# Kernel tuning notes

Hardware: AMD Instinct MI355X
Metric: run time of the kernel (lower is better)

## Reference

```python
import jax, jax.numpy as jnp
import numpy as np
import math

V, T, D_POI, D_OUT = 200000, 512, 256, 512
D_IN = D_POI + 4
D_HID = D_POI + 100


def setup_inputs() -> dict:
    key = jax.random.key(0)
    ks = jax.random.split(key, 12)
    s = 0.02
    return {
        "prev_poi_idx": jax.random.randint(ks[0], (T,), 0, V),
        "prev_time_frac": jax.random.uniform(ks[1], (T,), jnp.float32),
        "poi_final_emb": jax.random.normal(ks[2], (V, D_POI), jnp.float32),
        "poi_latlon_deg": jax.random.uniform(ks[3], (V, 2), jnp.float32) * 90.0,
        "ln_w": jnp.ones((D_IN,), jnp.float32),
        "ln_b": jnp.zeros((D_IN,), jnp.float32),
        "w1": jax.random.normal(ks[4], (D_IN, D_HID), jnp.float32) * s,
        "b1": jnp.zeros((D_HID,), jnp.float32),
        "w2": jax.random.normal(ks[5], (D_HID, D_POI), jnp.float32) * s,
        "b2": jnp.zeros((D_POI,), jnp.float32),
        "w_ih": jax.random.normal(ks[6], (3 * D_OUT, D_POI), jnp.float32) * s,
        "w_hh": jax.random.normal(ks[7], (3 * D_OUT, D_OUT), jnp.float32) * s,
        "b_ih": jnp.zeros((3 * D_OUT,), jnp.float32),
        "b_hh": jnp.zeros((3 * D_OUT,), jnp.float32),
        "q": jax.random.normal(ks[8], (D_OUT,), jnp.float32),
        "log_lam": jnp.array(0.0, jnp.float32),  # log(recency_lambda=1.0)
    }


def _haversine_km(lat1, lon1, lat2, lon2, eps=1e-12):
    dlat = (lat2 - lat1) * 0.5
    dlon = (lon2 - lon1) * 0.5
    a = jnp.sin(dlat) ** 2 + jnp.clip(jnp.cos(lat1), -1, 1) * jnp.clip(jnp.cos(lat2), -1, 1) * jnp.sin(dlon) ** 2
    c = 2.0 * jnp.arctan2(jnp.sqrt(jnp.clip(a, 0, 1)), jnp.sqrt(jnp.clip(1 - a, eps, 1)))
    return 6371.0088 * c


def _forward(prev_poi_idx, prev_time_frac, poi_final_emb, poi_latlon_deg,
             ln_w, ln_b, w1, b1, w2, b2, w_ih, w_hh, b_ih, b_hh, q, log_lam):
    Tn = prev_poi_idx.shape[0]
    poi_emb = poi_final_emb[prev_poi_idx]                       # (T, d_poi)
    t = jnp.clip(prev_time_frac, 0.0, 1.0)
    sin_t = jnp.sin(2.0 * math.pi * t)
    cos_t = jnp.cos(2.0 * math.pi * t)
    dif = jnp.mod(t[1:] - t[:-1], 1.0) * 24.0
    dt_h = jnp.concatenate([jnp.zeros((1,), t.dtype), dif])
    # _poi_radians is under no_grad in torch
    latlon = jax.lax.stop_gradient(poi_latlon_deg[prev_poi_idx])
    lat = jnp.deg2rad(jnp.clip(latlon[:, 0], -90, 90))
    lon = jnp.deg2rad(jnp.clip(latlon[:, 1], -180, 180))
    dd = _haversine_km(lat[:-1], lon[:-1], lat[1:], lon[1:])
    dd_km = jnp.concatenate([jnp.zeros((1,), dd.dtype), dd])
    feat = jnp.stack([sin_t, cos_t, jnp.log1p(dt_h), jnp.log1p(dd_km)], axis=-1)  # (T, 4)
    x = jnp.concatenate([poi_emb, feat], axis=-1)               # (T, d_poi+4)
    # fuse: LayerNorm -> Linear -> GELU -> (Dropout eval=id) -> Linear
    mu = jnp.mean(x, axis=-1, keepdims=True)
    var = jnp.mean((x - mu) ** 2, axis=-1, keepdims=True)
    x = (x - mu) * jax.lax.rsqrt(var + 1e-5) * ln_w + ln_b
    x = jax.nn.gelu(x @ w1 + b1, approximate=False) @ w2 + b2   # (T, d_poi)
    # GRU (single layer, unidirectional), torch gate order r,z,n
    gi_all = x @ w_ih.T + b_ih                                  # (T, 3H)
    def step(h, gi):
        gh = h @ w_hh.T + b_hh
        gi_r, gi_z, gi_n = jnp.split(gi, 3)
        gh_r, gh_z, gh_n = jnp.split(gh, 3)
        r = jax.nn.sigmoid(gi_r + gh_r)
        z = jax.nn.sigmoid(gi_z + gh_z)
        n = jnp.tanh(gi_n + r * gh_n)
        h_new = (1.0 - z) * n + z * h
        return h_new, h_new
    h0 = jnp.zeros((D_OUT,), x.dtype)
    _, hs = jax.lax.scan(step, h0, gi_all)                      # (T, d_out)
    D = hs.shape[-1]
    score = hs @ (q[:D] / jnp.sqrt(jnp.asarray(D, hs.dtype)))
    age = jnp.arange(Tn, dtype=hs.dtype)
    lam = jnp.maximum(jnp.exp(log_lam), 1e-4)
    score = score - lam * (Tn - 1 - age)
    attn = jax.nn.softmax(score, axis=0)
    summary = jnp.sum(attn[:, None] * hs, axis=0, keepdims=True)  # (1, d_out)
    return summary, attn


def reference(prev_poi_idx, prev_time_frac, poi_final_emb, poi_latlon_deg,
              ln_w, ln_b, w1, b1, w2, b2, w_ih, w_hh, b_ih, b_hh, q, log_lam):
    return _forward(prev_poi_idx, prev_time_frac, poi_final_emb, poi_latlon_deg,
                    ln_w, ln_b, w1, b1, w2, b2, w_ih, w_hh, b_ih, b_hh, q, log_lam)
```

## Files before the change

### kernel.cpp

```cpp
#include <hip/hip_runtime.h>
#include <math.h>

#define TT 512
#define DPOI 256
#define DIN 260
#define DHID 356
#define DOUTD 512
#define G3 1536

#define GB 8
#define HU (DOUTD / GB)
#define NRR (3 * HU)
#define NPAY DOUTD

__global__ __launch_bounds__(512)
void pre_kernel(const int* __restrict__ idx, const float* __restrict__ timef,
                const float* __restrict__ latlon, const float* __restrict__ emb,
                const float* __restrict__ lnw, const float* __restrict__ lnb,
                const float* __restrict__ w1, const float* __restrict__ b1,
                const float* __restrict__ w2, const float* __restrict__ b2,
                const float* __restrict__ wih, const float* __restrict__ bih,
                float* __restrict__ gi, unsigned* __restrict__ hcz) {
    int t = blockIdx.x;
    int tid = threadIdx.x;
    int wave = tid >> 6, lane = tid & 63;

    __shared__ float xl[DIN];
    __shared__ float h1l[DHID];
    __shared__ alignas(16) float x2l[DPOI];
    __shared__ float red[8];
    __shared__ float mu_s, rs_s;

    hcz[(size_t)t * 512 + tid] = 0u;

    float tv = fminf(fmaxf(timef[t], 0.f), 1.f);
    const float TWO_PI = 6.28318530717958647692f;
    float f0 = sinf(TWO_PI * tv);
    float f1 = cosf(TWO_PI * tv);
    float f2 = 0.f, f3 = 0.f;
    if (t > 0) {
        float tp = fminf(fmaxf(timef[t - 1], 0.f), 1.f);
        float d = tv - tp;
        d = d - floorf(d);
        f2 = log1pf(d * 24.f);
        int i0 = idx[t - 1], i1 = idx[t];
        float la0 = latlon[2 * (size_t)i0], lo0 = latlon[2 * (size_t)i0 + 1];
        float la1 = latlon[2 * (size_t)i1], lo1 = latlon[2 * (size_t)i1 + 1];
        const float D2R = 0.01745329251994329577f;
        float lat1 = fminf(fmaxf(la0, -90.f), 90.f) * D2R;
        float lon1 = fminf(fmaxf(lo0, -180.f), 180.f) * D2R;
        float lat2 = fminf(fmaxf(la1, -90.f), 90.f) * D2R;
        float lon2 = fminf(fmaxf(lo1, -180.f), 180.f) * D2R;
        float dlat = (lat2 - lat1) * 0.5f, dlon = (lon2 - lon1) * 0.5f;
        float sdlat = sinf(dlat), sdlon = sinf(dlon);
        float a = sdlat * sdlat +
                  fminf(fmaxf(cosf(lat1), -1.f), 1.f) * fminf(fmaxf(cosf(lat2), -1.f), 1.f) * sdlon * sdlon;
        float aa = fminf(fmaxf(a, 0.f), 1.f);
        float bb = fminf(fmaxf(1.f - a, 1e-12f), 1.f);
        float cc = 2.f * atan2f(sqrtf(aa), sqrtf(bb));
        f3 = log1pf(6371.0088f * cc);
    }
    float fv = (tid == 0) ? f0 : (tid == 1) ? f1 : (tid == 2) ? f2 : f3;

    float v0 = (tid < 256) ? emb[(size_t)idx[t] * DPOI + tid] : 0.f;
    float v1 = (tid < 4) ? fv : 0.f;

    float s = v0 + v1;
    for (int o = 32; o; o >>= 1) s += __shfl_down(s, o, 64);
    if (lane == 0) red[wave] = s;
    __syncthreads();
    if (tid == 0) {
        float mm = 0.f;
        for (int i = 0; i < 8; ++i) mm += red[i];
        mu_s = mm * (1.f / 260.f);
    }
    __syncthreads();
    float mu = mu_s;
    float d0 = (tid < 256) ? (v0 - mu) : 0.f;
    float d1 = (tid < 4) ? (v1 - mu) : 0.f;
    float sq = d0 * d0 + d1 * d1;
    for (int o = 32; o; o >>= 1) sq += __shfl_down(sq, o, 64);
    __syncthreads();
    if (lane == 0) red[wave] = sq;
    __syncthreads();
    if (tid == 0) {
        float vv = 0.f;
        for (int i = 0; i < 8; ++i) vv += red[i];
        rs_s = rsqrtf(vv * (1.f / 260.f) + 1e-5f);
    }
    __syncthreads();
    float rs = rs_s;
    if (tid < 256) xl[tid] = d0 * rs * lnw[tid] + lnb[tid];
    if (tid < 4)   xl[256 + tid] = d1 * rs * lnw[256 + tid] + lnb[256 + tid];
    __syncthreads();

    if (tid < DHID) {
        float acc = b1[tid];
        #pragma unroll 4
        for (int k = 0; k < DIN; ++k) acc = fmaf(xl[k], w1[k * DHID + tid], acc);
        h1l[tid] = 0.5f * acc * (1.f + erff(acc * 0.70710678118654752440f));
    }
    __syncthreads();

    if (tid < DPOI) {
        float acc = b2[tid];
        #pragma unroll 4
        for (int k = 0; k < DHID; ++k) acc = fmaf(h1l[k], w2[k * DPOI + tid], acc);
        x2l[tid] = acc;
    }
    __syncthreads();

    float4 xv = ((const float4*)x2l)[lane];
    for (int r = wave; r < G3; r += 8) {
        float4 wv = ((const float4*)(wih + (size_t)r * DPOI))[lane];
        float sd = xv.x * wv.x + xv.y * wv.y + xv.z * wv.z + xv.w * wv.w;
        for (int o = 32; o; o >>= 1) sd += __shfl_down(sd, o, 64);
        if (lane == 0) gi[(size_t)t * G3 + r] = sd + bih[r];
    }
}

__global__ __launch_bounds__(1024)
void gru_kernel(const float* __restrict__ gi, const float* __restrict__ whh,
                const float* __restrict__ bhh, float* __restrict__ hs,
                unsigned* __restrict__ hcomm) {
    __shared__ alignas(16) float hprev[DOUTD];
    __shared__ float gsum[NRR];

    int b = blockIdx.x;
    int tid = threadIdx.x;
    int wave = tid >> 6, lane = tid & 63;
    int jbase = b * HU;
    int g4 = lane >> 4, l4 = lane & 15;
    int rr0 = wave * 12 + g4 * 3;

    float4 wf0[8], wf1[8], wf2[8];
    float bl0, bl1, bl2;
    {
        int r0 = rr0, r1 = rr0 + 1, r2 = rr0 + 2;
        const float4* p0 = (const float4*)(whh + (size_t)((r0 >> 6) * DOUTD + jbase + (r0 & 63)) * DOUTD);
        const float4* p1 = (const float4*)(whh + (size_t)((r1 >> 6) * DOUTD + jbase + (r1 & 63)) * DOUTD);
        const float4* p2 = (const float4*)(whh + (size_t)((r2 >> 6) * DOUTD + jbase + (r2 & 63)) * DOUTD);
        #pragma unroll
        for (int m = 0; m < 8; ++m) {
            wf0[m] = p0[m * 16 + l4];
            wf1[m] = p1[m * 16 + l4];
            wf2[m] = p2[m * 16 + l4];
        }
        bl0 = bhh[(r0 >> 6) * DOUTD + jbase + (r0 & 63)];
        bl1 = bhh[(r1 >> 6) * DOUTD + jbase + (r1 & 63)];
        bl2 = bhh[(r2 >> 6) * DOUTD + jbase + (r2 & 63)];
    }
    if (tid < DOUTD) hprev[tid] = 0.f;
    __syncthreads();

    const float4* hp4 = (const float4*)hprev;
    long budget = 3000;

    float gir = 0.f, giz = 0.f, gin = 0.f, hreg = 0.f;
    if (tid < HU) {
        int j = jbase + tid;
        gir = gi[j];
        giz = gi[DOUTD + j];
        gin = gi[2 * DOUTD + j];
    }

    for (int s = 0; s < TT; ++s) {
        unsigned pa = 0, pb = 0;
        if (s > 0) {
            if (wave >= 4 && wave < 12 && (wave - 4) != b) {
                int u = ((wave - 4) << 6) + lane;
                const unsigned* ap = hcomm + (size_t)(s - 1) * NPAY + u;
                unsigned tag = (unsigned)s & 0xffffu;
                asm volatile("global_load_dword %0, %1, off sc0 sc1"
                             : "=v"(pa) : "v"(ap) : "memory");
                float xx = (float)(lane + 1) * 1e-6f;
                #pragma unroll
                for (int q = 0; q < 256; ++q) xx = fmaf(xx, 1.0000002f, 1.1920929e-7f);
                asm volatile("global_load_dword %0, %1, off sc0 sc1"
                             : "=v"(pb) : "v"(ap), "v"(xx) : "memory");
                do {
                    unsigned tmp; int scnt;
                    asm volatile(
                        "s_movk_i32 %[cnt], 64\n\t"
                        "1:\n\t"
                        "s_waitcnt vmcnt(1)\n\t"
                        "v_and_b32 %[t], 0xffff, %[pa]\n\t"
                        "v_cmp_ne_u32 vcc, %[tag], %[t]\n\t"
                        "s_cbranch_vccz 9f\n\t"
                        "global_load_dword %[pa], %[ptr], off sc0 sc1\n\t"
                        "s_waitcnt vmcnt(1)\n\t"
                        "v_and_b32 %[t], 0xffff, %[pb]\n\t"
                        "v_cmp_ne_u32 vcc, %[tag], %[t]\n\t"
                        "s_cbranch_vccz 8f\n\t"
                        "global_load_dword %[pb], %[ptr], off sc0 sc1\n\t"
                        "s_sub_u32 %[cnt], %[cnt], 1\n\t"
                        "s_cmp_lg_u32 %[cnt], 0\n\t"
                        "s_cbranch_scc1 1b\n\t"
                        "s_branch 9f\n\t"
                        "8:\n\t"
                        "v_mov_b32 %[pa], %[pb]\n\t"
                        "9:\n\t"
                        : [pa]"+v"(pa), [pb]"+v"(pb), [t]"=&v"(tmp), [cnt]"=&s"(scnt)
                        : [ptr]"v"(ap), [tag]"s"(tag)
                        : "vcc", "scc", "memory");
                    if ((pa & 0xffffu) == tag) break;
                } while (--budget > 0);
                hprev[u] = __uint_as_float(pa & 0xffff0000u);
            }
            __syncthreads();
            asm volatile("" :: "v"(pa), "v"(pb));
        }

        float a0 = 0.f, a1 = 0.f, a2 = 0.f;
        #pragma unroll
        for (int m = 0; m < 8; ++m) {
            float4 h4 = hp4[m * 16 + l4];
            a0 = fmaf(wf0[m].x, h4.x, a0); a0 = fmaf(wf0[m].y, h4.y, a0);
            a0 = fmaf(wf0[m].z, h4.z, a0); a0 = fmaf(wf0[m].w, h4.w, a0);
            a1 = fmaf(wf1[m].x, h4.x, a1); a1 = fmaf(wf1[m].y, h4.y, a1);
            a1 = fmaf(wf1[m].z, h4.z, a1); a1 = fmaf(wf1[m].w, h4.w, a1);
            a2 = fmaf(wf2[m].x, h4.x, a2); a2 = fmaf(wf2[m].y, h4.y, a2);
            a2 = fmaf(wf2[m].z, h4.z, a2); a2 = fmaf(wf2[m].w, h4.w, a2);
        }
        #pragma unroll
        for (int o = 1; o < 16; o <<= 1) {
            a0 += __shfl_xor(a0, o, 64);
            a1 += __shfl_xor(a1, o, 64);
            a2 += __shfl_xor(a2, o, 64);
        }
        if (l4 == 0) {
            gsum[rr0]     = a0 + bl0;
            gsum[rr0 + 1] = a1 + bl1;
            gsum[rr0 + 2] = a2 + bl2;
        }
        __syncthreads();

        if (tid < HU) {
            float gr  = gir + gsum[tid];
            float gz  = giz + gsum[HU + tid];
            float ghn = gsum[2 * HU + tid];
            float r = __builtin_amdgcn_rcpf(1.f + __expf(-gr));
            float z = __builtin_amdgcn_rcpf(1.f + __expf(-gz));
            float xt = gin + r * ghn;
            float n = 1.f - 2.f * __builtin_amdgcn_rcpf(__expf(2.f * xt) + 1.f);
            float hn = (1.f - z) * n + z * hreg;
            hreg = hn;
            unsigned ub = __float_as_uint(hn);
            ub += 0x7fffu + ((ub >> 16) & 1u);
            unsigned pay = (ub & 0xffff0000u) | ((unsigned)(s + 1) & 0xffffu);
            __hip_atomic_store(&hcomm[(size_t)s * NPAY + jbase + tid], pay,
                               __ATOMIC_RELAXED, __HIP_MEMORY_SCOPE_AGENT);
            int j = jbase + tid;
            hs[(size_t)s * DOUTD + j] = hn;
            hprev[j] = hn;
            if (s + 1 < TT) {
                const float* gn = gi + (size_t)(s + 1) * G3;
                gir = gn[j]; giz = gn[DOUTD + j]; gin = gn[2 * DOUTD + j];
            }
        }
    }
}

__global__ void attn_kernel(const float* __restrict__ hs, const float* __restrict__ q,
                            const float* __restrict__ log_lam, float* __restrict__ out) {
    int tid = threadIdx.x;
    int wave = tid >> 6, lane = tid & 63;
    __shared__ float sc[TT];
    __shared__ float at[TT];
    __shared__ float red[8];
    __shared__ float red2[8];
    __shared__ float denom_s, mx_s;

    const float qscale = 0.04419417382415921757f;
    for (int r = wave; r < TT; r += 8) {
        float acc = 0.f;
        #pragma unroll
        for (int m = 0; m < 8; ++m) {
            int k = lane + 64 * m;
            acc = fmaf(hs[(size_t)r * DOUTD + k], q[k], acc);
        }
        for (int o = 32; o; o >>= 1) acc += __shfl_down(acc, o, 64);
        if (lane == 0) sc[r] = acc * qscale;
    }
    __syncthreads();
    float lam = fmaxf(expf(log_lam[0]), 1e-4f);
    float s_i = sc[tid] - lam * (float)(TT - 1 - tid);

    float mval = s_i;
    for (int o = 32; o; o >>= 1) mval = fmaxf(mval, __shfl_down(mval, o, 64));
    if (lane == 0) red[wave] = mval;
    __syncthreads();
    if (tid == 0) {
        float mm = red[0];
        for (int i = 1; i < 8; ++i) mm = fmaxf(mm, red[i]);
        mx_s = mm;
    }
    __syncthreads();
    float e = expf(s_i - mx_s);
    float ssum = e;
    for (int o = 32; o; o >>= 1) ssum += __shfl_down(ssum, o, 64);
    if (lane == 0) red2[wave] = ssum;
    __syncthreads();
    if (tid == 0) {
        float dsum = 0.f;
        for (int i = 0; i < 8; ++i) dsum += red2[i];
        denom_s = dsum;
    }
    __syncthreads();
    float attn = e / denom_s;
    out[DOUTD + tid] = attn;
    at[tid] = attn;
    __syncthreads();
    float acc = 0.f;
    for (int i = 0; i < TT; ++i) acc = fmaf(at[i], hs[(size_t)i * DOUTD + tid], acc);
    out[tid] = acc;
}

extern "C" void kernel_launch(void* const* d_in, const int* in_sizes, int n_in,
                              void* d_out, int out_size, void* d_ws, size_t ws_size,
                              hipStream_t stream) {
    const int*   idx    = (const int*)d_in[0];
    const float* timef  = (const float*)d_in[1];
    const float* emb    = (const float*)d_in[2];
    const float* latlon = (const float*)d_in[3];
    const float* lnw    = (const float*)d_in[4];
    const float* lnb    = (const float*)d_in[5];
    const float* w1     = (const float*)d_in[6];
    const float* b1     = (const float*)d_in[7];
    const float* w2     = (const float*)d_in[8];
    const float* b2     = (const float*)d_in[9];
    const float* wih    = (const float*)d_in[10];
    const float* whh    = (const float*)d_in[11];
    const float* bih    = (const float*)d_in[12];
    const float* bhh    = (const float*)d_in[13];
    const float* q      = (const float*)d_in[14];
    const float* loglam = (const float*)d_in[15];
    float* out = (float*)d_out;

    unsigned* hcomm = (unsigned*)d_ws;
    float* gi = (float*)(hcomm + (size_t)TT * NPAY);
    float* hs = gi + (size_t)TT * G3;

    pre_kernel<<<TT, 512, 0, stream>>>(idx, timef, latlon, emb, lnw, lnb,
                                       w1, b1, w2, b2, wih, bih, gi, hcomm);
    gru_kernel<<<GB, 1024, 0, stream>>>(gi, whh, bhh, hs, hcomm);
    attn_kernel<<<1, TT, 0, stream>>>(hs, q, loglam, out);
}
```

Measured before the change: 1.536 ms.

## Fuse input projection and GRU into one kernel with per-step ready flags

Merges the per-timestep preprocessing (layernorm, MLP, input-gate projection) and the GRU recurrence into one launch. Blocks 0-7 run the recurrence while 256 extra blocks each produce two timesteps of gate inputs and publish per-step ready flags. The recurrence spins on a flag before reading each step's inputs, so preprocessing overlaps the serial scan instead of running before it. A separate init kernel zeroes the comm buffer and flags. This relies on the recurrence blocks and producer blocks being co-resident, uses bounded spin loops with a break that could read stale data, and adds waitcnt fixes in the polling asm.

```diff
diff --git a/kernel.cpp b/kernel.cpp
--- a/kernel.cpp
+++ b/kernel.cpp
@@ -12,123 +12,142 @@
 #define HU (DOUTD / GB)
 #define NRR (3 * HU)
 #define NPAY DOUTD
-
-__global__ __launch_bounds__(512)
-void pre_kernel(const int* __restrict__ idx, const float* __restrict__ timef,
-                const float* __restrict__ latlon, const float* __restrict__ emb,
-                const float* __restrict__ lnw, const float* __restrict__ lnb,
-                const float* __restrict__ w1, const float* __restrict__ b1,
-                const float* __restrict__ w2, const float* __restrict__ b2,
-                const float* __restrict__ wih, const float* __restrict__ bih,
-                float* __restrict__ gi, unsigned* __restrict__ hcz) {
-    int t = blockIdx.x;
+#define PREB 256
+#define NZ4 ((TT * NPAY + TT) / 4)
+
+__global__ void init_kernel(uint4* __restrict__ p) {
+    int i = blockIdx.x * blockDim.x + threadIdx.x;
+    int stride = gridDim.x * blockDim.x;
+    uint4 z; z.x = 0u; z.y = 0u; z.z = 0u; z.w = 0u;
+    for (; i < NZ4; i += stride) p[i] = z;
+}
+
+__global__ __launch_bounds__(1024)
+void mega_kernel(const int* __restrict__ idx, const float* __restrict__ timef,
+                 const float* __restrict__ latlon, const float* __restrict__ emb,
+                 const float* __restrict__ lnw, const float* __restrict__ lnb,
+                 const float* __restrict__ w1, const float* __restrict__ b1,
+                 const float* __restrict__ w2, const float* __restrict__ b2,
+                 const float* __restrict__ wih, const float* __restrict__ bih,
+                 const float* __restrict__ whh, const float* __restrict__ bhh,
+                 float* __restrict__ gi, float* __restrict__ hs,
+                 unsigned* __restrict__ hcomm, unsigned* __restrict__ ready) {
     int tid = threadIdx.x;
     int wave = tid >> 6, lane = tid & 63;
 
-    __shared__ float xl[DIN];
-    __shared__ float h1l[DHID];
-    __shared__ alignas(16) float x2l[DPOI];
-    __shared__ float red[8];
-    __shared__ float mu_s, rs_s;
-
-    hcz[(size_t)t * 512 + tid] = 0u;
-
-    float tv = fminf(fmaxf(timef[t], 0.f), 1.f);
-    const float TWO_PI = 6.28318530717958647692f;
-    float f0 = sinf(TWO_PI * tv);
-    float f1 = cosf(TWO_PI * tv);
-    float f2 = 0.f, f3 = 0.f;
-    if (t > 0) {
-        float tp = fminf(fmaxf(timef[t - 1], 0.f), 1.f);
-        float d = tv - tp;
-        d = d - floorf(d);
-        f2 = log1pf(d * 24.f);
-        int i0 = idx[t - 1], i1 = idx[t];
-        float la0 = latlon[2 * (size_t)i0], lo0 = latlon[2 * (size_t)i0 + 1];
-        float la1 = latlon[2 * (size_t)i1], lo1 = latlon[2 * (size_t)i1 + 1];
-        const float D2R = 0.01745329251994329577f;
-        float lat1 = fminf(fmaxf(la0, -90.f), 90.f) * D2R;
-        float lon1 = fminf(fmaxf(lo0, -180.f), 180.f) * D2R;
-        float lat2 = fminf(fmaxf(la1, -90.f), 90.f) * D2R;
-        float lon2 = fminf(fmaxf(lo1, -180.f), 180.f) * D2R;
-        float dlat = (lat2 - lat1) * 0.5f, dlon = (lon2 - lon1) * 0.5f;
-        float sdlat = sinf(dlat), sdlon = sinf(dlon);
-        float a = sdlat * sdlat +
-                  fminf(fmaxf(cosf(lat1), -1.f), 1.f) * fminf(fmaxf(cosf(lat2), -1.f), 1.f) * sdlon * sdlon;
-        float aa = fminf(fmaxf(a, 0.f), 1.f);
-        float bb = fminf(fmaxf(1.f - a, 1e-12f), 1.f);
-        float cc = 2.f * atan2f(sqrtf(aa), sqrtf(bb));
-        f3 = log1pf(6371.0088f * cc);
-    }
-    float fv = (tid == 0) ? f0 : (tid == 1) ? f1 : (tid == 2) ? f2 : f3;
-
-    float v0 = (tid < 256) ? emb[(size_t)idx[t] * DPOI + tid] : 0.f;
-    float v1 = (tid < 4) ? fv : 0.f;
-
-    float s = v0 + v1;
-    for (int o = 32; o; o >>= 1) s += __shfl_down(s, o, 64);
-    if (lane == 0) red[wave] = s;
-    __syncthreads();
-    if (tid == 0) {
-        float mm = 0.f;
-        for (int i = 0; i < 8; ++i) mm += red[i];
-        mu_s = mm * (1.f / 260.f);
-    }
-    __syncthreads();
-    float mu = mu_s;
-    float d0 = (tid < 256) ? (v0 - mu) : 0.f;
-    float d1 = (tid < 4) ? (v1 - mu) : 0.f;
-    float sq = d0 * d0 + d1 * d1;
-    for (int o = 32; o; o >>= 1) sq += __shfl_down(sq, o, 64);
-    __syncthreads();
-    if (lane == 0) red[wave] = sq;
-    __syncthreads();
-    if (tid == 0) {
-        float vv = 0.f;
-        for (int i = 0; i < 8; ++i) vv += red[i];
-        rs_s = rsqrtf(vv * (1.f / 260.f) + 1e-5f);
-    }
-    __syncthreads();
-    float rs = rs_s;
-    if (tid < 256) xl[tid] = d0 * rs * lnw[tid] + lnb[tid];
-    if (tid < 4)   xl[256 + tid] = d1 * rs * lnw[256 + tid] + lnb[256 + tid];
-    __syncthreads();
-
-    if (tid < DHID) {
-        float acc = b1[tid];
-        #pragma unroll 4
-        for (int k = 0; k < DIN; ++k) acc = fmaf(xl[k], w1[k * DHID + tid], acc);
-        h1l[tid] = 0.5f * acc * (1.f + erff(acc * 0.70710678118654752440f));
-    }
-    __syncthreads();
-
-    if (tid < DPOI) {
-        float acc = b2[tid];
-        #pragma unroll 4
-        for (int k = 0; k < DHID; ++k) acc = fmaf(h1l[k], w2[k * DPOI + tid], acc);
-        x2l[tid] = acc;
-    }
-    __syncthreads();
-
-    float4 xv = ((const float4*)x2l)[lane];
-    for (int r = wave; r < G3; r += 8) {
-        float4 wv = ((const float4*)(wih + (size_t)r * DPOI))[lane];
-        float sd = xv.x * wv.x + xv.y * wv.y + xv.z * wv.z + xv.w * wv.w;
-        for (int o = 32; o; o >>= 1) sd += __shfl_down(sd, o, 64);
-        if (lane == 0) gi[(size_t)t * G3 + r] = sd + bih[r];
-    }
-}
-
-__global__ __launch_bounds__(1024)
-void gru_kernel(const float* __restrict__ gi, const float* __restrict__ whh,
-                const float* __restrict__ bhh, float* __restrict__ hs,
-                unsigned* __restrict__ hcomm) {
+    if (blockIdx.x >= GB) {
+        __shared__ float xl[DIN];
+        __shared__ float h1l[DHID];
+        __shared__ alignas(16) float x2l[DPOI];
+        __shared__ float red[16];
+        __shared__ float mu_s, rs_s;
+        int pb = blockIdx.x - GB;
+
+        for (int half = 0; half < 2; ++half) {
+            int t = pb * 2 + half;
+
+            float fv = 0.f;
+            if (tid < 4) {
+                float tv = fminf(fmaxf(timef[t], 0.f), 1.f);
+                const float TWO_PI = 6.28318530717958647692f;
+                float f0 = sinf(TWO_PI * tv);
+                float f1 = cosf(TWO_PI * tv);
+                float f2 = 0.f, f3 = 0.f;
+                if (t > 0) {
+                    float tp = fminf(fmaxf(timef[t - 1], 0.f), 1.f);
+                    float d = tv - tp;
+                    d = d - floorf(d);
+                    f2 = log1pf(d * 24.f);
+                    int i0 = idx[t - 1], i1 = idx[t];
+                    float la0 = latlon[2 * (size_t)i0], lo0 = latlon[2 * (size_t)i0 + 1];
+                    float la1 = latlon[2 * (size_t)i1], lo1 = latlon[2 * (size_t)i1 + 1];
+                    const float D2R = 0.01745329251994329577f;
+                    float lat1 = fminf(fmaxf(la0, -90.f), 90.f) * D2R;
+                    float lon1 = fminf(fmaxf(lo0, -180.f), 180.f) * D2R;
+                    float lat2 = fminf(fmaxf(la1, -90.f), 90.f) * D2R;
+                    float lon2 = fminf(fmaxf(lo1, -180.f), 180.f) * D2R;
+                    float dlat = (lat2 - lat1) * 0.5f, dlon = (lon2 - lon1) * 0.5f;
+                    float sdlat = sinf(dlat), sdlon = sinf(dlon);
+                    float a = sdlat * sdlat +
+                              fminf(fmaxf(cosf(lat1), -1.f), 1.f) * fminf(fmaxf(cosf(lat2), -1.f), 1.f) * sdlon * sdlon;
+                    float aa = fminf(fmaxf(a, 0.f), 1.f);
+                    float bb = fminf(fmaxf(1.f - a, 1e-12f), 1.f);
+                    float cc = 2.f * atan2f(sqrtf(aa), sqrtf(bb));
+                    f3 = log1pf(6371.0088f * cc);
+                }
+                fv = (tid == 0) ? f0 : (tid == 1) ? f1 : (tid == 2) ? f2 : f3;
+            }
+
+            float v0 = (tid < 256) ? emb[(size_t)idx[t] * DPOI + tid] : 0.f;
+            float v1 = (tid < 4) ? fv : 0.f;
+
+            float s = v0 + v1;
+            for (int o = 32; o; o >>= 1) s += __shfl_down(s, o, 64);
+            if (lane == 0) red[wave] = s;
+            __syncthreads();
+            if (tid == 0) {
+                float mm = 0.f;
+                for (int i = 0; i < 16; ++i) mm += red[i];
+                mu_s = mm * (1.f / 260.f);
+            }
+            __syncthreads();
+            float mu = mu_s;
+            float d0 = (tid < 256) ? (v0 - mu) : 0.f;
+            float d1 = (tid < 4) ? (v1 - mu) : 0.f;
+            float sq = d0 * d0 + d1 * d1;
+            for (int o = 32; o; o >>= 1) sq += __shfl_down(sq, o, 64);
+            __syncthreads();
+            if (lane == 0) red[wave] = sq;
+            __syncthreads();
+            if (tid == 0) {
+                float vv = 0.f;
+                for (int i = 0; i < 16; ++i) vv += red[i];
+                rs_s = rsqrtf(vv * (1.f / 260.f) + 1e-5f);
+            }
+            __syncthreads();
+            float rs = rs_s;
+            if (tid < 256) xl[tid] = d0 * rs * lnw[tid] + lnb[tid];
+            if (tid < 4)   xl[256 + tid] = d1 * rs * lnw[256 + tid] + lnb[256 + tid];
+            __syncthreads();
+
+            if (tid < DHID) {
+                float acc = b1[tid];
+                #pragma unroll 4
+                for (int k = 0; k < DIN; ++k) acc = fmaf(xl[k], w1[k * DHID + tid], acc);
+                h1l[tid] = 0.5f * acc * (1.f + erff(acc * 0.70710678118654752440f));
+            }
+            __syncthreads();
+
+            if (tid < DPOI) {
+                float acc = b2[tid];
+                #pragma unroll 4
+                for (int k = 0; k < DHID; ++k) acc = fmaf(h1l[k], w2[k * DPOI + tid], acc);
+                x2l[tid] = acc;
+            }
+            __syncthreads();
+
+            float4 xv = ((const float4*)x2l)[lane];
+            for (int r = wave; r < G3; r += 16) {
+                float4 wv = ((const float4*)(wih + (size_t)r * DPOI))[lane];
+                float sd = xv.x * wv.x + xv.y * wv.y + xv.z * wv.z + xv.w * wv.w;
+                for (int o = 32; o; o >>= 1) sd += __shfl_down(sd, o, 64);
+                if (lane == 0)
+                    __hip_atomic_store(&gi[(size_t)t * G3 + r], sd + bih[r],
+                                       __ATOMIC_RELAXED, __HIP_MEMORY_SCOPE_AGENT);
+            }
+            __syncthreads();
+            if (tid == 0)
+                __hip_atomic_store(&ready[t], 1u, __ATOMIC_RELAXED,
+                                   __HIP_MEMORY_SCOPE_AGENT);
+            __syncthreads();
+        }
+        return;
+    }
+
     __shared__ alignas(16) float hprev[DOUTD];
     __shared__ float gsum[NRR];
 
     int b = blockIdx.x;
-    int tid = threadIdx.x;
-    int wave = tid >> 6, lane = tid & 63;
     int jbase = b * HU;
     int g4 = lane >> 4, l4 = lane & 15;
     int rr0 = wave * 12 + g4 * 3;
@@ -155,17 +174,22 @@
 
     const float4* hp4 = (const float4*)hprev;
     long budget = 3000;
+    long rbudget = 1000000;
 
     float gir = 0.f, giz = 0.f, gin = 0.f, hreg = 0.f;
     if (tid < HU) {
+        while (__hip_atomic_load(&ready[0], __ATOMIC_RELAXED,
+                                 __HIP_MEMORY_SCOPE_AGENT) == 0u) {
+            if (--rbudget < 0) break;
+        }
         int j = jbase + tid;
-        gir = gi[j];
-        giz = gi[DOUTD + j];
-        gin = gi[2 * DOUTD + j];
+        gir = __hip_atomic_load(&gi[j], __ATOMIC_RELAXED, __HIP_MEMORY_SCOPE_AGENT);
+        giz = __hip_atomic_load(&gi[DOUTD + j], __ATOMIC_RELAXED, __HIP_MEMORY_SCOPE_AGENT);
+        gin = __hip_atomic_load(&gi[2 * DOUTD + j], __ATOMIC_RELAXED, __HIP_MEMORY_SCOPE_AGENT);
     }
 
     for (int s = 0; s < TT; ++s) {
-        unsigned pa = 0, pb = 0;
+        unsigned pa = 0, pb2 = 0;
         if (s > 0) {
             if (wave >= 4 && wave < 12 && (wave - 4) != b) {
                 int u = ((wave - 4) << 6) + lane;
@@ -177,7 +201,7 @@
                 #pragma unroll
                 for (int q = 0; q < 256; ++q) xx = fmaf(xx, 1.0000002f, 1.1920929e-7f);
                 asm volatile("global_load_dword %0, %1, off sc0 sc1"
-                             : "=v"(pb) : "v"(ap), "v"(xx) : "memory");
+                             : "=v"(pb2) : "v"(ap), "v"(xx) : "memory");
                 do {
                     unsigned tmp; int scnt;
                     asm volatile(
@@ -198,17 +222,19 @@
                         "s_cbranch_scc1 1b\n\t"
                         "s_branch 9f\n\t"
                         "8:\n\t"
+                        "s_waitcnt vmcnt(0)\n\t"
                         "v_mov_b32 %[pa], %[pb]\n\t"
                         "9:\n\t"
-                        : [pa]"+v"(pa), [pb]"+v"(pb), [t]"=&v"(tmp), [cnt]"=&s"(scnt)
+                        : [pa]"+v"(pa), [pb]"+v"(pb2), [t]"=&v"(tmp), [cnt]"=&s"(scnt)
                         : [ptr]"v"(ap), [tag]"s"(tag)
                         : "vcc", "scc", "memory");
                     if ((pa & 0xffffu) == tag) break;
                 } while (--budget > 0);
+                asm volatile("s_waitcnt vmcnt(0)" ::: "memory");
                 hprev[u] = __uint_as_float(pa & 0xffff0000u);
             }
             __syncthreads();
-            asm volatile("" :: "v"(pa), "v"(pb));
+            asm volatile("" :: "v"(pa), "v"(pb2));
         }
 
         float a0 = 0.f, a1 = 0.f, a2 = 0.f;
@@ -254,8 +280,14 @@
             hs[(size_t)s * DOUTD + j] = hn;
             hprev[j] = hn;
             if (s + 1 < TT) {
+                while (__hip_atomic_load(&ready[s + 1], __ATOMIC_RELAXED,
+                                         __HIP_MEMORY_SCOPE_AGENT) == 0u) {
+                    if (--rbudget < 0) break;
+                }
                 const float* gn = gi + (size_t)(s + 1) * G3;
-                gir = gn[j]; giz = gn[DOUTD + j]; gin = gn[2 * DOUTD + j];
+                gir = __hip_atomic_load(&gn[j], __ATOMIC_RELAXED, __HIP_MEMORY_SCOPE_AGENT);
+                giz = __hip_atomic_load(&gn[DOUTD + j], __ATOMIC_RELAXED, __HIP_MEMORY_SCOPE_AGENT);
+                gin = __hip_atomic_load(&gn[2 * DOUTD + j], __ATOMIC_RELAXED, __HIP_MEMORY_SCOPE_AGENT);
             }
         }
     }
@@ -338,11 +370,13 @@
     float* out = (float*)d_out;
 
     unsigned* hcomm = (unsigned*)d_ws;
-    float* gi = (float*)(hcomm + (size_t)TT * NPAY);
+    unsigned* ready = hcomm + (size_t)TT * NPAY;
+    float* gi = (float*)(ready + TT);
     float* hs = gi + (size_t)TT * G3;
 
-    pre_kernel<<<TT, 512, 0, stream>>>(idx, timef, latlon, emb, lnw, lnb,
-                                       w1, b1, w2, b2, wih, bih, gi, hcomm);
-    gru_kernel<<<GB, 1024, 0, stream>>>(gi, whh, bhh, hs, hcomm);
+    init_kernel<<<256, 256, 0, stream>>>((uint4*)d_ws);
+    mega_kernel<<<GB + PREB, 1024, 0, stream>>>(idx, timef, latlon, emb, lnw, lnb,
+                                                w1, b1, w2, b2, wih, bih, whh, bhh,
+                                                gi, hs, hcomm, ready);
     attn_kernel<<<1, TT, 0, stream>>>(hs, q, loglam, out);
 }
```

Measured after the change: 2.096 ms. 1.36x slower.

## Split GRU across 16 blocks and fuse attention into the GRU kernel

Applied to the files above, without the earlier changes.

Doubles the number of cooperating GRU blocks from 8 to 16. Each block now owns 32 hidden units, and the per-thread recurrent weight slice is halved, so each step does less serial dot-product work. The separate attention launch is folded into the GRU kernel: block 0 waits on per-block done flags and then computes the softmax and summary. This removes one kernel launch. The cost is more cross-block polling traffic per step, extra waitcnt fences, and a spin-wait whose correctness depends on every block being co-resident.

```diff
diff --git a/kernel.cpp b/kernel.cpp
--- a/kernel.cpp
+++ b/kernel.cpp
@@ -8,7 +8,7 @@
 #define DOUTD 512
 #define G3 1536
 
-#define GB 8
+#define GB 16
 #define HU (DOUTD / GB)
 #define NRR (3 * HU)
 #define NPAY DOUTD
@@ -20,7 +20,8 @@
                 const float* __restrict__ w1, const float* __restrict__ b1,
                 const float* __restrict__ w2, const float* __restrict__ b2,
                 const float* __restrict__ wih, const float* __restrict__ bih,
-                float* __restrict__ gi, unsigned* __restrict__ hcz) {
+                float* __restrict__ gi, unsigned* __restrict__ hcz,
+                unsigned* __restrict__ done) {
     int t = blockIdx.x;
     int tid = threadIdx.x;
     int wave = tid >> 6, lane = tid & 63;
@@ -32,6 +33,7 @@
     __shared__ float mu_s, rs_s;
 
     hcz[(size_t)t * 512 + tid] = 0u;
+    if (t == 0 && tid < 64) done[tid] = 0u;
 
     float tv = fminf(fmaxf(timef[t], 0.f), 1.f);
     const float TWO_PI = 6.28318530717958647692f;
@@ -120,35 +122,42 @@
 }
 
 __global__ __launch_bounds__(1024)
-void gru_kernel(const float* __restrict__ gi, const float* __restrict__ whh,
-                const float* __restrict__ bhh, float* __restrict__ hs,
-                unsigned* __restrict__ hcomm) {
+void gru_attn_kernel(const float* __restrict__ gi, const float* __restrict__ whh,
+                     const float* __restrict__ bhh, float* __restrict__ hs,
+                     unsigned* __restrict__ hcomm, unsigned* __restrict__ done,
+                     const float* __restrict__ q, const float* __restrict__ log_lam,
+                     float* __restrict__ out) {
     __shared__ alignas(16) float hprev[DOUTD];
     __shared__ float gsum[NRR];
+    __shared__ float sc[TT];
+    __shared__ float at[TT];
+    __shared__ float red[8];
+    __shared__ float red2[8];
+    __shared__ float denom_s, mx_s;
 
     int b = blockIdx.x;
     int tid = threadIdx.x;
     int wave = tid >> 6, lane = tid & 63;
     int jbase = b * HU;
-    int g4 = lane >> 4, l4 = lane & 15;
-    int rr0 = wave * 12 + g4 * 3;
-
-    float4 wf0[8], wf1[8], wf2[8];
+    int g2 = lane >> 5, l5 = lane & 31;
+    int rr0 = wave * 6 + g2 * 3;
+
+    float4 wf0[4], wf1[4], wf2[4];
     float bl0, bl1, bl2;
     {
         int r0 = rr0, r1 = rr0 + 1, r2 = rr0 + 2;
-        const float4* p0 = (const float4*)(whh + (size_t)((r0 >> 6) * DOUTD + jbase + (r0 & 63)) * DOUTD);
-        const float4* p1 = (const float4*)(whh + (size_t)((r1 >> 6) * DOUTD + jbase + (r1 & 63)) * DOUTD);
-        const float4* p2 = (const float4*)(whh + (size_t)((r2 >> 6) * DOUTD + jbase + (r2 & 63)) * DOUTD);
+        const float4* p0 = (const float4*)(whh + (size_t)((r0 >> 5) * DOUTD + jbase + (r0 & 31)) * DOUTD);
+        const float4* p1 = (const float4*)(whh + (size_t)((r1 >> 5) * DOUTD + jbase + (r1 & 31)) * DOUTD);
+        const float4* p2 = (const float4*)(whh + (size_t)((r2 >> 5) * DOUTD + jbase + (r2 & 31)) * DOUTD);
         #pragma unroll
-        for (int m = 0; m < 8; ++m) {
-            wf0[m] = p0[m * 16 + l4];
-            wf1[m] = p1[m * 16 + l4];
-            wf2[m] = p2[m * 16 + l4];
-        }
-        bl0 = bhh[(r0 >> 6) * DOUTD + jbase + (r0 & 63)];
-        bl1 = bhh[(r1 >> 6) * DOUTD + jbase + (r1 & 63)];
-        bl2 = bhh[(r2 >> 6) * DOUTD + jbase + (r2 & 63)];
+        for (int m = 0; m < 4; ++m) {
+            wf0[m] = p0[m * 32 + l5];
+            wf1[m] = p1[m * 32 + l5];
+            wf2[m] = p2[m * 32 + l5];
+        }
+        bl0 = bhh[(r0 >> 5) * DOUTD + jbase + (r0 & 31)];
+        bl1 = bhh[(r1 >> 5) * DOUTD + jbase + (r1 & 31)];
+        bl2 = bhh[(r2 >> 5) * DOUTD + jbase + (r2 & 31)];
     }
     if (tid < DOUTD) hprev[tid] = 0.f;
     __syncthreads();
@@ -165,19 +174,20 @@
     }
 
     for (int s = 0; s < TT; ++s) {
-        unsigned pa = 0, pb = 0;
+        unsigned pa = 0, pb2 = 0;
         if (s > 0) {
-            if (wave >= 4 && wave < 12 && (wave - 4) != b) {
-                int u = ((wave - 4) << 6) + lane;
+            bool poller = (wave >= 4 && wave < 12);
+            int u = ((wave - 4) << 6) + lane;
+            if (poller && (u >> 5) != b) {
                 const unsigned* ap = hcomm + (size_t)(s - 1) * NPAY + u;
                 unsigned tag = (unsigned)s & 0xffffu;
                 asm volatile("global_load_dword %0, %1, off sc0 sc1"
                              : "=v"(pa) : "v"(ap) : "memory");
                 float xx = (float)(lane + 1) * 1e-6f;
                 #pragma unroll
-                for (int q = 0; q < 256; ++q) xx = fmaf(xx, 1.0000002f, 1.1920929e-7f);
+                for (int qq = 0; qq < 256; ++qq) xx = fmaf(xx, 1.0000002f, 1.1920929e-7f);
                 asm volatile("global_load_dword %0, %1, off sc0 sc1"
-                             : "=v"(pb) : "v"(ap), "v"(xx) : "memory");
+                             : "=v"(pb2) : "v"(ap), "v"(xx) : "memory");
                 do {
                     unsigned tmp; int scnt;
                     asm volatile(
@@ -198,23 +208,25 @@
                         "s_cbranch_scc1 1b\n\t"
                         "s_branch 9f\n\t"
                         "8:\n\t"
+                        "s_waitcnt vmcnt(0)\n\t"
                         "v_mov_b32 %[pa], %[pb]\n\t"
                         "9:\n\t"
-                        : [pa]"+v"(pa), [pb]"+v"(pb), [t]"=&v"(tmp), [cnt]"=&s"(scnt)
+                        : [pa]"+v"(pa), [pb]"+v"(pb2), [t]"=&v"(tmp), [cnt]"=&s"(scnt)
                         : [ptr]"v"(ap), [tag]"s"(tag)
                         : "vcc", "scc", "memory");
                     if ((pa & 0xffffu) == tag) break;
                 } while (--budget > 0);
+                asm volatile("s_waitcnt vmcnt(0)" ::: "memory");
                 hprev[u] = __uint_as_float(pa & 0xffff0000u);
             }
             __syncthreads();
-            asm volatile("" :: "v"(pa), "v"(pb));
+            asm volatile("" :: "v"(pa), "v"(pb2));
         }
 
         float a0 = 0.f, a1 = 0.f, a2 = 0.f;
         #pragma unroll
-        for (int m = 0; m < 8; ++m) {
-            float4 h4 = hp4[m * 16 + l4];
+        for (int m = 0; m < 4; ++m) {
+            float4 h4 = hp4[m * 32 + l5];
             a0 = fmaf(wf0[m].x, h4.x, a0); a0 = fmaf(wf0[m].y, h4.y, a0);
             a0 = fmaf(wf0[m].z, h4.z, a0); a0 = fmaf(wf0[m].w, h4.w, a0);
             a1 = fmaf(wf1[m].x, h4.x, a1); a1 = fmaf(wf1[m].y, h4.y, a1);
@@ -223,12 +235,12 @@
             a2 = fmaf(wf2[m].z, h4.z, a2); a2 = fmaf(wf2[m].w, h4.w, a2);
         }
         #pragma unroll
-        for (int o = 1; o < 16; o <<= 1) {
+        for (int o = 1; o < 32; o <<= 1) {
             a0 += __shfl_xor(a0, o, 64);
             a1 += __shfl_xor(a1, o, 64);
             a2 += __shfl_xor(a2, o, 64);
         }
-        if (l4 == 0) {
+        if (l5 == 0) {
             gsum[rr0]     = a0 + bl0;
             gsum[rr0 + 1] = a1 + bl1;
             gsum[rr0 + 2] = a2 + bl2;
@@ -251,7 +263,8 @@
             __hip_atomic_store(&hcomm[(size_t)s * NPAY + jbase + tid], pay,
                                __ATOMIC_RELAXED, __HIP_MEMORY_SCOPE_AGENT);
             int j = jbase + tid;
-            hs[(size_t)s * DOUTD + j] = hn;
+            __hip_atomic_store(&hs[(size_t)s * DOUTD + j], hn,
+                               __ATOMIC_RELAXED, __HIP_MEMORY_SCOPE_AGENT);
             hprev[j] = hn;
             if (s + 1 < TT) {
                 const float* gn = gi + (size_t)(s + 1) * G3;
@@ -259,20 +272,26 @@
             }
         }
     }
-}
-
-__global__ void attn_kernel(const float* __restrict__ hs, const float* __restrict__ q,
-                            const float* __restrict__ log_lam, float* __restrict__ out) {
-    int tid = threadIdx.x;
-    int wave = tid >> 6, lane = tid & 63;
-    __shared__ float sc[TT];
-    __shared__ float at[TT];
-    __shared__ float red[8];
-    __shared__ float red2[8];
-    __shared__ float denom_s, mx_s;
+
+    asm volatile("s_waitcnt vmcnt(0)" ::: "memory");
+    __syncthreads();
+    if (tid == 0)
+        __hip_atomic_store(&done[b], 1u, __ATOMIC_RELAXED, __HIP_MEMORY_SCOPE_AGENT);
+    if (b != 0) return;
+
+    {
+        long dbud = 20L * 1000 * 1000;
+        if (tid < GB) {
+            while (__hip_atomic_load(&done[tid], __ATOMIC_RELAXED,
+                                     __HIP_MEMORY_SCOPE_AGENT) == 0u) {
+                if (--dbud < 0) break;
+            }
+        }
+        __syncthreads();
+    }
 
     const float qscale = 0.04419417382415921757f;
-    for (int r = wave; r < TT; r += 8) {
+    for (int r = wave; r < TT; r += 16) {
         float acc = 0.f;
         #pragma unroll
         for (int m = 0; m < 8; ++m) {
@@ -284,11 +303,11 @@
     }
     __syncthreads();
     float lam = fmaxf(expf(log_lam[0]), 1e-4f);
-    float s_i = sc[tid] - lam * (float)(TT - 1 - tid);
+    float s_i = (tid < TT) ? (sc[tid] - lam * (float)(TT - 1 - tid)) : -1e30f;
 
     float mval = s_i;
     for (int o = 32; o; o >>= 1) mval = fmaxf(mval, __shfl_down(mval, o, 64));
-    if (lane == 0) red[wave] = mval;
+    if (lane == 0 && wave < 8) red[wave] = mval;
     __syncthreads();
     if (tid == 0) {
         float mm = red[0];
@@ -296,10 +315,10 @@
         mx_s = mm;
     }
     __syncthreads();
-    float e = expf(s_i - mx_s);
+    float e = (tid < TT) ? expf(s_i - mx_s) : 0.f;
     float ssum = e;
     for (int o = 32; o; o >>= 1) ssum += __shfl_down(ssum, o, 64);
-    if (lane == 0) red2[wave] = ssum;
+    if (lane == 0 && wave < 8) red2[wave] = ssum;
     __syncthreads();
     if (tid == 0) {
         float dsum = 0.f;
@@ -307,13 +326,17 @@
         denom_s = dsum;
     }
     __syncthreads();
-    float attn = e / denom_s;
-    out[DOUTD + tid] = attn;
-    at[tid] = attn;
-    __syncthreads();
-    float acc = 0.f;
-    for (int i = 0; i < TT; ++i) acc = fmaf(at[i], hs[(size_t)i * DOUTD + tid], acc);
-    out[tid] = acc;
+    if (tid < TT) {
+        float attn = e / denom_s;
+        out[DOUTD + tid] = attn;
+        at[tid] = attn;
+    }
+    __syncthreads();
+    if (tid < TT) {
+        float acc = 0.f;
+        for (int i = 0; i < TT; ++i) acc = fmaf(at[i], hs[(size_t)i * DOUTD + tid], acc);
+        out[tid] = acc;
+    }
 }
 
 extern "C" void kernel_launch(void* const* d_in, const int* in_sizes, int n_in,
@@ -338,11 +361,12 @@
     float* out = (float*)d_out;
 
     unsigned* hcomm = (unsigned*)d_ws;
-    float* gi = (float*)(hcomm + (size_t)TT * NPAY);
+    unsigned* done  = hcomm + (size_t)TT * NPAY;
+    float* gi = (float*)(done + 64);
     float* hs = gi + (size_t)TT * G3;
 
     pre_kernel<<<TT, 512, 0, stream>>>(idx, timef, latlon, emb, lnw, lnb,
-                                       w1, b1, w2, b2, wih, bih, gi, hcomm);
-    gru_kernel<<<GB, 1024, 0, stream>>>(gi, whh, bhh, hs, hcomm);
-    attn_kernel<<<1, TT, 0, stream>>>(hs, q, loglam, out);
+                                       w1, b1, w2, b2, wih, bih, gi, hcomm, done);
+    gru_attn_kernel<<<GB, 1024, 0, stream>>>(gi, whh, bhh, hs, hcomm, done,
+                                             q, loglam, out);
 }
```

Measured after the change: 1.541 ms. Within noise of the previous version (+0.3%).
